# Performance work log

Measured on AMD Instinct MI355X. Metric: run time of the kernel, lower is better.

Reference implementation:

```python
import jax, jax.numpy as jnp
import numpy as np

D_MODEL = 256
D_INNER = 512
D_STATE = 16
DT_RANK = 16
D_CONV = 4
N_LAYERS = 2
EPS = 1e-5
SEQ_LEN = 16384
IN_DIM = 32
OUT_DIM = 1


def _layernorm(x, g, b):
    m = jnp.mean(x, axis=-1, keepdims=True)
    v = jnp.mean((x - m) ** 2, axis=-1, keepdims=True)
    return (x - m) * jax.lax.rsqrt(v + EPS) * g + b


def _rmsnorm(x, w):
    return x * jax.lax.rsqrt(jnp.mean(x * x, axis=-1, keepdims=True) + EPS) * w


def _selective_scan(x, delta, A, B, C, D):
    # x, delta: (B,L,ED); A: (ED,N); B,C: (B,L,N); D: (ED,)
    dA = jnp.exp(delta[..., None] * A)                    # (B,L,ED,N)
    dBx = (delta * x)[..., None] * B[:, :, None, :]       # (B,L,ED,N)

    def comb(l, r):
        al, bl = l
        ar, br = r
        return (al * ar, bl * ar + br)

    _, hs = jax.lax.associative_scan(comb, (dA, dBx), axis=1)  # (B,L,ED,N)
    y = jnp.einsum('blen,bln->ble', hs, C) + x * D
    return y


def _mamba_block(u, rms_w, inW, convW, convB, xpW, dtW, dtB, A_log, Dp, outW):
    h = _rmsnorm(u, rms_w)
    xz = h @ inW                                   # (B,L,2*ED)
    xin, z = jnp.split(xz, 2, axis=-1)
    # depthwise causal conv1d over time
    xc = jax.lax.conv_general_dilated(
        jnp.transpose(xin, (0, 2, 1)), convW,
        window_strides=(1,), padding=[(D_CONV - 1, 0)],
        feature_group_count=D_INNER,
        dimension_numbers=('NCH', 'OIH', 'NCH')) + convB[None, :, None]
    xs = jax.nn.silu(jnp.transpose(xc, (0, 2, 1)))  # (B,L,ED)
    dbc = xs @ xpW                                  # (B,L,dt_rank+2N)
    delta = jax.nn.softplus(dbc[..., :DT_RANK] @ dtW + dtB)
    Bm = dbc[..., DT_RANK:DT_RANK + D_STATE]
    Cm = dbc[..., DT_RANK + D_STATE:]
    y = _selective_scan(xs, delta, -jnp.exp(A_log), Bm, Cm, Dp)
    out = (y * jax.nn.silu(z)) @ outW
    return u + out  # residual


def _forward(x, W_in, b_in, ln1_g, ln1_b,
             rms_w, inW, convW, convB, xpW, dtW, dtB, A_log, Dp, outW,
             ln2_g, ln2_b, W1, b1, ln3_g, ln3_b, W2, b2):
    # input_proj (dropout = identity in eval)
    h = jax.nn.gelu(_layernorm(x[0] @ W_in + b_in, ln1_g, ln1_b))
    h = h[None]  # (1,L,D)
    for i in range(N_LAYERS):
        h = _mamba_block(h, rms_w[i], inW[i], convW[i], convB[i], xpW[i],
                         dtW[i], dtB[i], A_log[i], Dp[i], outW[i])
    # output_proj
    h = _layernorm(h, ln2_g, ln2_b)
    h = jax.nn.gelu(h @ W1 + b1)
    h = _layernorm(h, ln3_g, ln3_b)
    h = jnp.tanh(h @ W2 + b2)
    return h.reshape(-1)


def setup_inputs() -> dict:
    key = jax.random.key(0)
    ks = jax.random.split(key, 16)
    s = 0.02
    A = jnp.tile(jnp.arange(1, D_STATE + 1, dtype=jnp.float32)[None, :], (D_INNER, 1))
    return {
        'x': jax.random.normal(ks[0], (1, SEQ_LEN, IN_DIM), jnp.float32),
        'W_in': s * jax.random.normal(ks[1], (IN_DIM, D_MODEL), jnp.float32),
        'b_in': jnp.zeros((D_MODEL,), jnp.float32),
        'ln1_g': jnp.ones((D_MODEL,), jnp.float32),
        'ln1_b': jnp.zeros((D_MODEL,), jnp.float32),
        'rms_w': jnp.ones((N_LAYERS, D_MODEL), jnp.float32),
        'inW': s * jax.random.normal(ks[2], (N_LAYERS, D_MODEL, 2 * D_INNER), jnp.float32),
        'convW': s * jax.random.normal(ks[3], (N_LAYERS, D_INNER, 1, D_CONV), jnp.float32),
        'convB': jnp.zeros((N_LAYERS, D_INNER), jnp.float32),
        'xpW': s * jax.random.normal(ks[4], (N_LAYERS, D_INNER, DT_RANK + 2 * D_STATE), jnp.float32),
        'dtW': s * jax.random.normal(ks[5], (N_LAYERS, DT_RANK, D_INNER), jnp.float32),
        'dtB': 0.1 * jax.random.normal(ks[6], (N_LAYERS, D_INNER), jnp.float32),
        'A_log': jnp.tile(jnp.log(A)[None], (N_LAYERS, 1, 1)),
        'Dp': jnp.ones((N_LAYERS, D_INNER), jnp.float32),
        'outW': s * jax.random.normal(ks[7], (N_LAYERS, D_INNER, D_MODEL), jnp.float32),
        'ln2_g': jnp.ones((D_MODEL,), jnp.float32),
        'ln2_b': jnp.zeros((D_MODEL,), jnp.float32),
        'W1': s * jax.random.normal(ks[8], (D_MODEL, D_MODEL // 2), jnp.float32),
        'b1': jnp.zeros((D_MODEL // 2,), jnp.float32),
        'ln3_g': jnp.ones((D_MODEL // 2,), jnp.float32),
        'ln3_b': jnp.zeros((D_MODEL // 2,), jnp.float32),
        'W2': s * jax.random.normal(ks[9], (D_MODEL // 2, OUT_DIM), jnp.float32),
        'b2': jnp.zeros((OUT_DIM,), jnp.float32),
    }


def reference(x, W_in, b_in, ln1_g, ln1_b, rms_w, inW, convW, convB, xpW,
              dtW, dtB, A_log, Dp, outW, ln2_g, ln2_b, W1, b1, ln3_g, ln3_b,
              W2, b2):
    return _forward(x, W_in, b_in, ln1_g, ln1_b, rms_w, inW, convW, convB,
                    xpW, dtW, dtB, A_log, Dp, outW, ln2_g, ln2_b, W1, b1,
                    ln3_g, ln3_b, W2, b2)
```

## Files before the change

kernel.cpp:

```cpp
#include <hip/hip_runtime.h>
#include <hip/hip_bf16.h>
#include <math.h>

#define L_SEQ 16384
#define DM 256
#define DI 512
#define DS 16
#define NCH 512
#define CHL 32
#define CLB 16

typedef __attribute__((ext_vector_type(8))) short short8v;
typedef __attribute__((ext_vector_type(4))) float f32x4;

__device__ __forceinline__ float tanh_fast(float x){
  float xc = fminf(x, 15.f);
  float t = __expf(2.f*xc);
  return (t-1.f)/(t+1.f);
}
__device__ __forceinline__ float gelu_f(float x){
  float x3 = x*x*x;
  return 0.5f*x*(1.0f + tanh_fast(0.7978845608028654f*(x + 0.044715f*x3)));
}
__device__ __forceinline__ float silu_f(float x){
  return x / (1.0f + __expf(-x));
}
__device__ __forceinline__ float softplus_f(float x){
  return fmaxf(x,0.0f) + __logf(1.0f + __expf(-fabsf(x)));
}
__device__ __forceinline__ float bf2f(unsigned short u){
  return __uint_as_float(((unsigned int)u)<<16);
}
__device__ __forceinline__ void gload16(const void* g, void* l){
  __builtin_amdgcn_global_load_lds((const __attribute__((address_space(1))) void*)g,
                                   (__attribute__((address_space(3))) void*)l, 16, 0, 0);
}

__device__ __forceinline__ void powers16(float r, float* dA){
  float r2 = r*r;
  float r4 = r2*r2;
  float r8 = r4*r4;
  dA[0]=r;        dA[1]=r2;       dA[2]=r2*r;     dA[3]=r4;
  dA[4]=r4*r;     dA[5]=r4*r2;    dA[6]=r4*dA[2]; dA[7]=r8;
  dA[8]=r8*r;     dA[9]=r8*r2;    dA[10]=r8*dA[2];dA[11]=r8*r4;
  dA[12]=r8*dA[4];dA[13]=r8*dA[5];dA[14]=r8*dA[6];dA[15]=r8*r8;
}

__global__ void k_cvtw(const float* __restrict__ inW, const float* __restrict__ outW,
                       const float* __restrict__ W1, __hip_bfloat16* __restrict__ inWt,
                       __hip_bfloat16* __restrict__ outWt, __hip_bfloat16* __restrict__ W1t){
  int idx = blockIdx.x*256 + threadIdx.x;
  if(idx < 524288){
    int layer = idx >> 18;
    int r = idx & 262143;
    int n = r >> 8, k = r & 255;
    inWt[idx] = __float2bfloat16(inW[layer*262144 + k*1024 + n]);
  } else if(idx < 786432){
    int j = idx - 524288;
    int layer = j >> 17;
    int r = j & 131071;
    int n = r >> 9, k = r & 511;
    outWt[j] = __float2bfloat16(outW[layer*131072 + k*256 + n]);
  } else if(idx < 819200){
    int j = idx - 786432;
    int n = j >> 8, k = j & 255;
    W1t[j] = __float2bfloat16(W1[k*128 + n]);
  }
}

__global__ void k_wd(const float* __restrict__ xpW, const float* __restrict__ dtW,
                     __hip_bfloat16* __restrict__ Wd_t, __hip_bfloat16* __restrict__ Wbc_t){
  int idx = blockIdx.x*256 + threadIdx.x;
  if(idx < 524288){
    int layer = idx >> 18;
    int r = idx & 262143;
    int n = r >> 9, k = r & 511;
    const float* xp = xpW + layer*512*48;
    const float* dt = dtW + layer*16*512;
    float s = 0.f;
#pragma unroll
    for(int j=0;j<16;j++) s = fmaf(xp[k*48+j], dt[j*512+n], s);
    Wd_t[idx] = __float2bfloat16(s);
  } else if(idx < 655360){
    int j2 = idx - 524288;
    int layer = j2 >> 16;
    int r = j2 & 65535;
    int n = r >> 9, k = r & 511;
    float v = (n < 32) ? xpW[layer*512*48 + k*48 + 16 + n] : 0.f;
    Wbc_t[j2] = __float2bfloat16(v);
  }
}

__global__ __launch_bounds__(256) void k_input(const float* __restrict__ x,
                        const float* __restrict__ Win, const float* __restrict__ bin,
                        const float* __restrict__ g, const float* __restrict__ b,
                        __hip_bfloat16* __restrict__ u){
  int wv = threadIdx.x>>6, lane = threadIdx.x&63;
  int r = blockIdx.x*4 + wv;
  int c0 = lane*4;
  float acc[4];
  { float4 bv = *(const float4*)&bin[c0];
    acc[0]=bv.x; acc[1]=bv.y; acc[2]=bv.z; acc[3]=bv.w; }
#pragma unroll
  for(int k=0;k<32;k++){
    float xk = x[r*32+k];
    float4 wv4 = *(const float4*)&Win[k*DM+c0];
    acc[0]=fmaf(xk,wv4.x,acc[0]); acc[1]=fmaf(xk,wv4.y,acc[1]);
    acc[2]=fmaf(xk,wv4.z,acc[2]); acc[3]=fmaf(xk,wv4.w,acc[3]);
  }
  float s = (acc[0]+acc[1])+(acc[2]+acc[3]);
  float sq = acc[0]*acc[0]+acc[1]*acc[1]+acc[2]*acc[2]+acc[3]*acc[3];
#pragma unroll
  for(int o=32;o;o>>=1){ s += __shfl_xor(s,o); sq += __shfl_xor(sq,o); }
  float mean = s*(1.0f/DM);
  float var = sq*(1.0f/DM) - mean*mean;
  float rs = rsqrtf(var+1e-5f);
  float4 gv = *(const float4*)&g[c0];
  float4 bv = *(const float4*)&b[c0];
  __hip_bfloat16 ob[4] = {
    __float2bfloat16(gelu_f((acc[0]-mean)*rs*gv.x+bv.x)),
    __float2bfloat16(gelu_f((acc[1]-mean)*rs*gv.y+bv.y)),
    __float2bfloat16(gelu_f((acc[2]-mean)*rs*gv.z+bv.z)),
    __float2bfloat16(gelu_f((acc[3]-mean)*rs*gv.w+bv.w))};
  *(uint2*)&u[r*DM+c0] = *(uint2*)ob;
}

__global__ __launch_bounds__(256) void k_rms(const __hip_bfloat16* __restrict__ u,
                      const float* __restrict__ w, __hip_bfloat16* __restrict__ o){
  int wv = threadIdx.x>>6, lane = threadIdx.x&63;
  int r = blockIdx.x*4 + wv;
  int c0 = lane*4;
  ushort4 uv = *(const ushort4*)&u[r*DM+c0];
  float v0=bf2f(uv.x), v1=bf2f(uv.y), v2=bf2f(uv.z), v3=bf2f(uv.w);
  float sq = v0*v0+v1*v1+v2*v2+v3*v3;
#pragma unroll
  for(int s=32;s;s>>=1) sq += __shfl_xor(sq,s);
  float rs = rsqrtf(sq*(1.0f/DM)+1e-5f);
  float4 wv4 = *(const float4*)&w[c0];
  __hip_bfloat16 ob[4] = {
    __float2bfloat16(v0*rs*wv4.x), __float2bfloat16(v1*rs*wv4.y),
    __float2bfloat16(v2*rs*wv4.z), __float2bfloat16(v3*rs*wv4.w)};
  *(uint2*)&o[r*DM+c0] = *(uint2*)ob;
}

__global__ __launch_bounds__(256) void k_ln(const __hip_bfloat16* __restrict__ u,
                     const float* __restrict__ g, const float* __restrict__ b,
                     __hip_bfloat16* __restrict__ o){
  int wv = threadIdx.x>>6, lane = threadIdx.x&63;
  int r = blockIdx.x*4 + wv;
  int c0 = lane*4;
  ushort4 uv = *(const ushort4*)&u[r*DM+c0];
  float v[4] = {bf2f(uv.x), bf2f(uv.y), bf2f(uv.z), bf2f(uv.w)};
  float s = (v[0]+v[1])+(v[2]+v[3]);
  float sq = v[0]*v[0]+v[1]*v[1]+v[2]*v[2]+v[3]*v[3];
#pragma unroll
  for(int o2=32;o2;o2>>=1){ s += __shfl_xor(s,o2); sq += __shfl_xor(sq,o2); }
  float mean = s*(1.0f/DM);
  float var = sq*(1.0f/DM) - mean*mean;
  float rs = rsqrtf(var+1e-5f);
  float4 gv = *(const float4*)&g[c0];
  float4 bv = *(const float4*)&b[c0];
  __hip_bfloat16 ob[4] = {
    __float2bfloat16((v[0]-mean)*rs*gv.x+bv.x),
    __float2bfloat16((v[1]-mean)*rs*gv.y+bv.y),
    __float2bfloat16((v[2]-mean)*rs*gv.z+bv.z),
    __float2bfloat16((v[3]-mean)*rs*gv.w+bv.w)};
  *(uint2*)&o[r*DM+c0] = *(uint2*)ob;
}

template<int EPI, typename OT>
__global__ __launch_bounds__(512) void k_mgemm(const __hip_bfloat16* __restrict__ A,
    const __hip_bfloat16* __restrict__ Wt, const float* __restrict__ bias,
    const OT* __restrict__ R, OT* __restrict__ C, int M, int K, int ldc, int Nout){
  __shared__ char lds[69632];
  short* As = (short*)lds;
  short* Bs = (short*)(lds + 32768);
  float* Ob = (float*)lds;
  int t = threadIdx.x, lane = t&63, wave = t>>6;
  int gx = gridDim.x;
  int f = blockIdx.y*gx + blockIdx.x;
  int s = f >> 3;
  int sy = s/gx;
  int yb = (f&7)*(gridDim.y>>3) + sy;
  int xb = s - sy*gx;
  int m0 = yb*128, n0 = xb*128;
  int wm = (wave>>1)*32, wn = (wave&1)*64;
  f32x4 acc[2][4] = {};
  int nk = K >> 7;
  for(int ki=0; ki<nk; ki++){
    int kt = ki<<7;
    __syncthreads();
#pragma unroll
    for(int c=0;c<4;c++){
      int off = c*8192 + t*16;
      int row = off>>8;
      int sl  = ((off>>4)&15) ^ (row&15);
      gload16(&A [(m0+row)*K + kt + sl*8], (char*)As + off);
      gload16(&Wt[(n0+row)*K + kt + sl*8], (char*)Bs + off);
    }
    asm volatile("s_waitcnt vmcnt(0)" ::: "memory");
    __syncthreads();
#pragma unroll
    for(int ks=0; ks<4; ks++){
      short8v a[2], b[4];
      int k8 = ks*4 + (lane>>4);
#pragma unroll
      for(int i=0;i<2;i++){
        int lr = wm + i*16 + (lane&15);
        a[i] = *(const short8v*)&As[lr*128 + (k8 ^ (lr&15))*8];
      }
#pragma unroll
      for(int j=0;j<4;j++){
        int lr = wn + j*16 + (lane&15);
        b[j] = *(const short8v*)&Bs[lr*128 + (k8 ^ (lr&15))*8];
      }
#pragma unroll
      for(int i=0;i<2;i++)
#pragma unroll
        for(int j=0;j<4;j++)
          acc[i][j] = __builtin_amdgcn_mfma_f32_16x16x32_bf16(a[i], b[j], acc[i][j], 0,0,0);
    }
  }
  __syncthreads();
#pragma unroll
  for(int i=0;i<2;i++){
    int r0 = wm + i*16 + (lane>>4)*4;
#pragma unroll
    for(int j=0;j<4;j++){
      int cl = wn + j*16 + (lane&15);
#pragma unroll
      for(int r=0;r<4;r++) Ob[(r0+r)*132 + cl] = acc[i][j][r];
    }
  }
  __syncthreads();
#pragma unroll
  for(int v=0; v<8; v++){
    int fidx = (t*8+v)*4;
    int row = fidx>>7, col = fidx&127;
    if(col < Nout){
      float4 o = *(const float4*)&Ob[row*132 + col];
      int grow = m0 + row, gcol = n0 + col;
      if(EPI==1){
        if constexpr(sizeof(OT)==2){
          ushort4 rv = *(const ushort4*)&R[grow*ldc+gcol];
          o.x+=bf2f(rv.x); o.y+=bf2f(rv.y); o.z+=bf2f(rv.z); o.w+=bf2f(rv.w);
        } else {
          float4 rv = *(const float4*)&R[grow*ldc+gcol];
          o.x+=rv.x; o.y+=rv.y; o.z+=rv.z; o.w+=rv.w;
        }
      }
      if(EPI==2){
        float4 bv = *(const float4*)&bias[gcol];
        o.x=gelu_f(o.x+bv.x); o.y=gelu_f(o.y+bv.y);
        o.z=gelu_f(o.z+bv.z); o.w=gelu_f(o.w+bv.w);
      }
      if(EPI==3){
        float4 bv = *(const float4*)&bias[gcol];
        o.x=softplus_f(o.x+bv.x); o.y=softplus_f(o.y+bv.y);
        o.z=softplus_f(o.z+bv.z); o.w=softplus_f(o.w+bv.w);
      }
      if constexpr(sizeof(OT)==2){
        __hip_bfloat16 ob[4] = {__float2bfloat16(o.x),__float2bfloat16(o.y),
                                __float2bfloat16(o.z),__float2bfloat16(o.w)};
        *(uint2*)&C[grow*ldc+gcol] = *(uint2*)ob;
      } else {
        *(float4*)&C[grow*ldc+gcol] = o;
      }
    }
  }
}

__global__ __launch_bounds__(256) void k_conv(const __hip_bfloat16* __restrict__ xz,
                       const float* __restrict__ cw, const float* __restrict__ cb,
                       __hip_bfloat16* __restrict__ xs_bf){
  int idx = blockIdx.x*256 + threadIdx.x;
  int cg = idx & 127, lb = idx >> 7;
  int c4 = cg*4;
  int l0 = lb*CLB;
  float w[4][4], bias[4];
#pragma unroll
  for(int j=0;j<4;j++){
    float4 wv = *(const float4*)&cw[(c4+j)*4];
    w[j][0]=wv.x; w[j][1]=wv.y; w[j][2]=wv.z; w[j][3]=wv.w;
  }
  { float4 bv = *(const float4*)&cb[c4];
    bias[0]=bv.x; bias[1]=bv.y; bias[2]=bv.z; bias[3]=bv.w; }
  float xm0[4], xm1[4], xm2[4];
#pragma unroll
  for(int j=0;j<4;j++){ xm0[j]=0.f; xm1[j]=0.f; xm2[j]=0.f; }
  if(l0 >= 3){
    ushort4 r0 = *(const ushort4*)&xz[(l0-3)*1024 + c4];
    ushort4 r1 = *(const ushort4*)&xz[(l0-2)*1024 + c4];
    ushort4 r2 = *(const ushort4*)&xz[(l0-1)*1024 + c4];
    xm0[0]=bf2f(r0.x); xm0[1]=bf2f(r0.y); xm0[2]=bf2f(r0.z); xm0[3]=bf2f(r0.w);
    xm1[0]=bf2f(r1.x); xm1[1]=bf2f(r1.y); xm1[2]=bf2f(r1.z); xm1[3]=bf2f(r1.w);
    xm2[0]=bf2f(r2.x); xm2[1]=bf2f(r2.y); xm2[2]=bf2f(r2.z); xm2[3]=bf2f(r2.w);
  }
#pragma unroll 4
  for(int l=l0; l<l0+CLB; l++){
    ushort4 rc = *(const ushort4*)&xz[l*1024 + c4];
    float xc[4] = {bf2f(rc.x), bf2f(rc.y), bf2f(rc.z), bf2f(rc.w)};
    __hip_bfloat16 ob[4];
#pragma unroll
    for(int j=0;j<4;j++){
      float acc = bias[j];
      acc = fmaf(xm0[j], w[j][0], acc);
      acc = fmaf(xm1[j], w[j][1], acc);
      acc = fmaf(xm2[j], w[j][2], acc);
      acc = fmaf(xc[j],  w[j][3], acc);
      ob[j] = __float2bfloat16(silu_f(acc));
    }
    *(uint2*)&xs_bf[l*DI + c4] = *(uint2*)ob;
#pragma unroll
    for(int j=0;j<4;j++){ xm0[j]=xm1[j]; xm1[j]=xm2[j]; xm2[j]=xc[j]; }
  }
}

__global__ __launch_bounds__(256) void k_scan1(const __hip_bfloat16* __restrict__ delta,
                        const __hip_bfloat16* __restrict__ xs,
                        const float* __restrict__ dbc32, const float* __restrict__ A_log,
                        float* __restrict__ Atot, float* __restrict__ Btot){
  __shared__ float bcs[CHL*32];
  int t = threadIdx.x;
  int chunk = blockIdx.x >> 1;
  int e = ((blockIdx.x & 1) << 8) + t;
  int l0 = chunk*CHL;
  ((float4*)bcs)[t] = ((const float4*)&dbc32[l0*32])[t];
  float A[16];
  {
    const float4* al = (const float4*)&A_log[e*DS];
#pragma unroll
    for(int q=0;q<4;q++){
      float4 a = al[q];
      A[q*4+0] = -__expf(a.x); A[q*4+1] = -__expf(a.y);
      A[q*4+2] = -__expf(a.z); A[q*4+3] = -__expf(a.w);
    }
  }
  bool pf = true;
#pragma unroll
  for(int n=1;n<16;n++) pf = pf && (fabsf(A[n] - (n+1)*A[0]) <= 1e-4f*fabsf(A[n]));
  float carry[16], aprod[16];
#pragma unroll
  for(int n=0;n<16;n++){ carry[n]=0.f; aprod[n]=1.f; }
  __syncthreads();
  if(pf){
    float A0 = A[0];
#pragma unroll 2
    for(int li=0; li<CHL; li++){
      int l = l0 + li;
      float d  = bf2f(*(const unsigned short*)&delta[l*DI+e]);
      float xv = bf2f(*(const unsigned short*)&xs[l*DI+e]);
      float dxv = d*xv;
      const float4* bp = (const float4*)&bcs[li*32];
      float4 b0=bp[0], b1=bp[1], b2=bp[2], b3=bp[3];
      float B[16] = {b0.x,b0.y,b0.z,b0.w, b1.x,b1.y,b1.z,b1.w,
                     b2.x,b2.y,b2.z,b2.w, b3.x,b3.y,b3.z,b3.w};
      float r = __expf(d*A0);
      float dA[16]; powers16(r, dA);
#pragma unroll
      for(int n=0;n<16;n++){
        carry[n] = fmaf(carry[n], dA[n], dxv*B[n]);
        aprod[n] *= dA[n];
      }
    }
  } else {
#pragma unroll 2
    for(int li=0; li<CHL; li++){
      int l = l0 + li;
      float d  = bf2f(*(const unsigned short*)&delta[l*DI+e]);
      float xv = bf2f(*(const unsigned short*)&xs[l*DI+e]);
      float dxv = d*xv;
      const float4* bp = (const float4*)&bcs[li*32];
      float4 b0=bp[0], b1=bp[1], b2=bp[2], b3=bp[3];
      float B[16] = {b0.x,b0.y,b0.z,b0.w, b1.x,b1.y,b1.z,b1.w,
                     b2.x,b2.y,b2.z,b2.w, b3.x,b3.y,b3.z,b3.w};
#pragma unroll
      for(int n=0;n<16;n++){
        float dA = __expf(d*A[n]);
        carry[n] = fmaf(carry[n], dA, dxv*B[n]);
        aprod[n] *= dA;
      }
    }
  }
  float4* ap = (float4*)&Atot[chunk*8192 + e*DS];
  float4* bp = (float4*)&Btot[chunk*8192 + e*DS];
#pragma unroll
  for(int q=0;q<4;q++){
    ap[q] = make_float4(aprod[q*4],aprod[q*4+1],aprod[q*4+2],aprod[q*4+3]);
    bp[q] = make_float4(carry[q*4],carry[q*4+1],carry[q*4+2],carry[q*4+3]);
  }
}

__global__ void k_scan2(const float* __restrict__ Atot, const float* __restrict__ Btot,
                        float* __restrict__ h0){
  int tg = blockIdx.x*256 + threadIdx.x;
  float carry = 0.f;
  for(int c=0;c<NCH;c++){
    float a = Atot[c*8192+tg];
    float b = Btot[c*8192+tg];
    h0[c*8192+tg] = carry;
    carry = fmaf(carry, a, b);
  }
}

__global__ __launch_bounds__(256) void k_scan3(const __hip_bfloat16* __restrict__ delta,
                        const __hip_bfloat16* __restrict__ xs,
                        const float* __restrict__ dbc32, const float* __restrict__ A_log,
                        const float* __restrict__ Dp, const float* __restrict__ h0,
                        const __hip_bfloat16* __restrict__ xz, __hip_bfloat16* __restrict__ y){
  __shared__ float bcs[CHL*32];
  int t = threadIdx.x;
  int chunk = blockIdx.x >> 1;
  int e = ((blockIdx.x & 1) << 8) + t;
  int l0 = chunk*CHL;
  ((float4*)bcs)[t] = ((const float4*)&dbc32[l0*32])[t];
  float A[16];
  {
    const float4* al = (const float4*)&A_log[e*DS];
#pragma unroll
    for(int q=0;q<4;q++){
      float4 a = al[q];
      A[q*4+0] = -__expf(a.x); A[q*4+1] = -__expf(a.y);
      A[q*4+2] = -__expf(a.z); A[q*4+3] = -__expf(a.w);
    }
  }
  bool pf = true;
#pragma unroll
  for(int n=1;n<16;n++) pf = pf && (fabsf(A[n] - (n+1)*A[0]) <= 1e-4f*fabsf(A[n]));
  float carry[16];
  {
    const float4* hp = (const float4*)&h0[chunk*8192 + e*DS];
#pragma unroll
    for(int q=0;q<4;q++){
      float4 h = hp[q];
      carry[q*4+0]=h.x; carry[q*4+1]=h.y; carry[q*4+2]=h.z; carry[q*4+3]=h.w;
    }
  }
  float Dv = Dp[e];
  __syncthreads();
  if(pf){
    float A0 = A[0];
#pragma unroll 2
    for(int li=0; li<CHL; li++){
      int l = l0 + li;
      float d  = bf2f(*(const unsigned short*)&delta[l*DI+e]);
      float xv = bf2f(*(const unsigned short*)&xs[l*DI+e]);
      float dxv = d*xv;
      const float4* bp = (const float4*)&bcs[li*32];
      float4 b0=bp[0], b1=bp[1], b2=bp[2], b3=bp[3];
      float4 c0=bp[4], c1=bp[5], c2=bp[6], c3=bp[7];
      float B[16] = {b0.x,b0.y,b0.z,b0.w, b1.x,b1.y,b1.z,b1.w,
                     b2.x,b2.y,b2.z,b2.w, b3.x,b3.y,b3.z,b3.w};
      float Cv[16] = {c0.x,c0.y,c0.z,c0.w, c1.x,c1.y,c1.z,c1.w,
                      c2.x,c2.y,c2.z,c2.w, c3.x,c3.y,c3.z,c3.w};
      float r = __expf(d*A0);
      float dA[16]; powers16(r, dA);
      float p[4] = {0.f,0.f,0.f,0.f};
#pragma unroll
      for(int n=0;n<16;n++){
        carry[n] = fmaf(carry[n], dA[n], dxv*B[n]);
        p[n&3] = fmaf(carry[n], Cv[n], p[n&3]);
      }
      float ps = (p[0]+p[1]) + (p[2]+p[3]);
      float z = bf2f(*(const unsigned short*)&xz[l*1024 + 512 + e]);
      y[l*DI+e] = __float2bfloat16(fmaf(xv, Dv, ps) * silu_f(z));
    }
  } else {
#pragma unroll 2
    for(int li=0; li<CHL; li++){
      int l = l0 + li;
      float d  = bf2f(*(const unsigned short*)&delta[l*DI+e]);
      float xv = bf2f(*(const unsigned short*)&xs[l*DI+e]);
      float dxv = d*xv;
      const float4* bp = (const float4*)&bcs[li*32];
      float4 b0=bp[0], b1=bp[1], b2=bp[2], b3=bp[3];
      float4 c0=bp[4], c1=bp[5], c2=bp[6], c3=bp[7];
      float B[16] = {b0.x,b0.y,b0.z,b0.w, b1.x,b1.y,b1.z,b1.w,
                     b2.x,b2.y,b2.z,b2.w, b3.x,b3.y,b3.z,b3.w};
      float Cv[16] = {c0.x,c0.y,c0.z,c0.w, c1.x,c1.y,c1.z,c1.w,
                      c2.x,c2.y,c2.z,c2.w, c3.x,c3.y,c3.z,c3.w};
      float p[4] = {0.f,0.f,0.f,0.f};
#pragma unroll
      for(int n=0;n<16;n++){
        float dA = __expf(d*A[n]);
        carry[n] = fmaf(carry[n], dA, dxv*B[n]);
        p[n&3] = fmaf(carry[n], Cv[n], p[n&3]);
      }
      float ps = (p[0]+p[1]) + (p[2]+p[3]);
      float z = bf2f(*(const unsigned short*)&xz[l*1024 + 512 + e]);
      y[l*DI+e] = __float2bfloat16(fmaf(xv, Dv, ps) * silu_f(z));
    }
  }
}

__global__ void k_final(const float* __restrict__ h2, const float* __restrict__ g,
                        const float* __restrict__ b, const float* __restrict__ W2,
                        const float* __restrict__ b2, float* __restrict__ out){
  int lane = threadIdx.x&63;
  int wv = threadIdx.x>>6;
  int r = blockIdx.x*4 + wv;
  float v0 = h2[r*128+lane], v1 = h2[r*128+64+lane];
  float s = v0+v1, sq = v0*v0+v1*v1;
#pragma unroll
  for(int o=32;o;o>>=1){ s += __shfl_xor(s,o); sq += __shfl_xor(sq,o); }
  float mean = s*(1.0f/128), var = sq*(1.0f/128) - mean*mean;
  float rs = rsqrtf(var+1e-5f);
  float n0 = (v0-mean)*rs*g[lane]+b[lane];
  float n1 = (v1-mean)*rs*g[lane+64]+b[lane+64];
  float d = n0*W2[lane] + n1*W2[lane+64];
#pragma unroll
  for(int o=32;o;o>>=1) d += __shfl_xor(d,o);
  if(lane==0) out[r] = tanhf(d + b2[0]);
}

extern "C" void kernel_launch(void* const* d_in, const int* in_sizes, int n_in,
                              void* d_out, int out_size, void* d_ws, size_t ws_size,
                              hipStream_t stream){
  const float* x    = (const float*)d_in[0];
  const float* Win  = (const float*)d_in[1];
  const float* bin  = (const float*)d_in[2];
  const float* ln1g = (const float*)d_in[3];
  const float* ln1b = (const float*)d_in[4];
  const float* rmsw = (const float*)d_in[5];
  const float* inW  = (const float*)d_in[6];
  const float* convW= (const float*)d_in[7];
  const float* convB= (const float*)d_in[8];
  const float* xpW  = (const float*)d_in[9];
  const float* dtW  = (const float*)d_in[10];
  const float* dtB  = (const float*)d_in[11];
  const float* A_log= (const float*)d_in[12];
  const float* Dp   = (const float*)d_in[13];
  const float* outW = (const float*)d_in[14];
  const float* ln2g = (const float*)d_in[15];
  const float* ln2b = (const float*)d_in[16];
  const float* W1   = (const float*)d_in[17];
  const float* b1   = (const float*)d_in[18];
  const float* ln3g = (const float*)d_in[19];
  const float* ln3b = (const float*)d_in[20];
  const float* W2   = (const float*)d_in[21];
  const float* b2   = (const float*)d_in[22];
  float* out = (float*)d_out;
  float* ws = (float*)d_ws;
  __hip_bfloat16* u_bf = (__hip_bfloat16*)ws;
  __hip_bfloat16* hn_bf = (__hip_bfloat16*)(ws + 4194304);
  __hip_bfloat16* xz_bf = (__hip_bfloat16*)(ws + 8388608);
  float* dbc32 = ws + 16777216;
  __hip_bfloat16* delta_bf = (__hip_bfloat16*)(ws + 17301504);
  __hip_bfloat16* y_bf  = (__hip_bfloat16*)(ws + 25690112);
  __hip_bfloat16* xs_bf = (__hip_bfloat16*)(ws + 29884416);
  float* Atot  = ws + 34078720;
  float* Btot  = ws + 38273024;
  float* h0    = Btot;
  float* h2    = ws;
  __hip_bfloat16* inWt   = (__hip_bfloat16*)(ws + 42467328);
  __hip_bfloat16* outWt  = (__hip_bfloat16*)(ws + 42729472);
  __hip_bfloat16* W1t    = (__hip_bfloat16*)(ws + 42860544);
  __hip_bfloat16* Wd_t   = (__hip_bfloat16*)(ws + 42876928);
  __hip_bfloat16* Wbc_t  = (__hip_bfloat16*)(ws + 43139072);

  k_cvtw<<<3200,256,0,stream>>>(inW, outW, W1, inWt, outWt, W1t);
  k_wd<<<2560,256,0,stream>>>(xpW, dtW, Wd_t, Wbc_t);
  k_input<<<L_SEQ/4,256,0,stream>>>(x,Win,bin,ln1g,ln1b,u_bf);
  for(int i=0;i<2;i++){
    k_rms<<<L_SEQ/4,256,0,stream>>>(u_bf, rmsw+i*DM, hn_bf);
    k_mgemm<0,__hip_bfloat16><<<dim3(8, L_SEQ/128),512,0,stream>>>(hn_bf, inWt+i*262144, nullptr, nullptr, xz_bf, L_SEQ, DM, 1024, 1024);
    k_conv<<<(L_SEQ/CLB)*128/256,256,0,stream>>>(xz_bf, convW+i*DI*4, convB+i*DI, xs_bf);
    k_mgemm<3,__hip_bfloat16><<<dim3(4, L_SEQ/128),512,0,stream>>>(xs_bf, Wd_t+i*262144, dtB+i*DI, nullptr, delta_bf, L_SEQ, DI, 512, 512);
    k_mgemm<0,float><<<dim3(1, L_SEQ/128),512,0,stream>>>(xs_bf, Wbc_t+i*65536, nullptr, nullptr, dbc32, L_SEQ, DI, 32, 32);
    k_scan1<<<NCH*2,256,0,stream>>>(delta_bf, xs_bf, dbc32, A_log+i*DI*DS, Atot, Btot);
    k_scan2<<<32,256,0,stream>>>(Atot, Btot, h0);
    k_scan3<<<NCH*2,256,0,stream>>>(delta_bf, xs_bf, dbc32, A_log+i*DI*DS, Dp+i*DI, h0, xz_bf, y_bf);
    k_mgemm<1,__hip_bfloat16><<<dim3(2, L_SEQ/128),512,0,stream>>>(y_bf, outWt+i*131072, nullptr, u_bf, u_bf, L_SEQ, DI, 256, 256);
  }
  k_ln<<<L_SEQ/4,256,0,stream>>>(u_bf, ln2g, ln2b, hn_bf);
  k_mgemm<2,float><<<dim3(1, L_SEQ/128),512,0,stream>>>(hn_bf, W1t, b1, nullptr, h2, L_SEQ, DM, 128, 128);
  k_final<<<L_SEQ/4,256,0,stream>>>(h2, ln3g, ln3b, W2, b2, out);
}
```

Before: 445.2 us.

## Fuse RMSNorm into in-proj GEMM via row sum-of-squares and merge delta/BC GEMMs

Removes the standalone RMSNorm kernel. The norm weight is folded into the in-projection weights, and per-row sums of squares are produced by the input kernel and by the first out-projection epilogue using atomics. The in-proj GEMM then scales each row by rsqrt. The delta and B/C projections are merged into one GEMM with a split epilogue, the two weight-prep kernels are combined, and the scan2 carry loop batches its loads in groups of eight. This trades an extra atomic pass and zero-fill against fewer kernel launches and less activation traffic.

New measurement: 413.0 us. -7.2%, faster.

```diff
diff --git a/kernel.cpp b/kernel.cpp
--- a/kernel.cpp
+++ b/kernel.cpp
@@ -46,15 +46,17 @@
   dA[12]=r8*dA[4];dA[13]=r8*dA[5];dA[14]=r8*dA[6];dA[15]=r8*r8;
 }
 
-__global__ void k_cvtw(const float* __restrict__ inW, const float* __restrict__ outW,
-                       const float* __restrict__ W1, __hip_bfloat16* __restrict__ inWt,
-                       __hip_bfloat16* __restrict__ outWt, __hip_bfloat16* __restrict__ W1t){
+__global__ void k_prep(const float* __restrict__ inW, const float* __restrict__ rmsw,
+                       const float* __restrict__ outW, const float* __restrict__ W1,
+                       const float* __restrict__ xpW, const float* __restrict__ dtW,
+                       __hip_bfloat16* __restrict__ inWt, __hip_bfloat16* __restrict__ outWt,
+                       __hip_bfloat16* __restrict__ W1t, __hip_bfloat16* __restrict__ Wdbc_t){
   int idx = blockIdx.x*256 + threadIdx.x;
   if(idx < 524288){
     int layer = idx >> 18;
     int r = idx & 262143;
     int n = r >> 8, k = r & 255;
-    inWt[idx] = __float2bfloat16(inW[layer*262144 + k*1024 + n]);
+    inWt[idx] = __float2bfloat16(inW[layer*262144 + k*1024 + n] * rmsw[layer*256+k]);
   } else if(idx < 786432){
     int j = idx - 524288;
     int layer = j >> 17;
@@ -65,36 +67,34 @@
     int j = idx - 786432;
     int n = j >> 8, k = j & 255;
     W1t[j] = __float2bfloat16(W1[k*128 + n]);
-  }
-}
-
-__global__ void k_wd(const float* __restrict__ xpW, const float* __restrict__ dtW,
-                     __hip_bfloat16* __restrict__ Wd_t, __hip_bfloat16* __restrict__ Wbc_t){
-  int idx = blockIdx.x*256 + threadIdx.x;
-  if(idx < 524288){
-    int layer = idx >> 18;
-    int r = idx & 262143;
+  } else if(idx < 1474560){
+    int j = idx - 819200;
+    int layer = j / 327680;
+    int r = j % 327680;
     int n = r >> 9, k = r & 511;
     const float* xp = xpW + layer*512*48;
-    const float* dt = dtW + layer*16*512;
-    float s = 0.f;
-#pragma unroll
-    for(int j=0;j<16;j++) s = fmaf(xp[k*48+j], dt[j*512+n], s);
-    Wd_t[idx] = __float2bfloat16(s);
-  } else if(idx < 655360){
-    int j2 = idx - 524288;
-    int layer = j2 >> 16;
-    int r = j2 & 65535;
-    int n = r >> 9, k = r & 511;
-    float v = (n < 32) ? xpW[layer*512*48 + k*48 + 16 + n] : 0.f;
-    Wbc_t[j2] = __float2bfloat16(v);
-  }
+    float v;
+    if(n < 512){
+      const float* dt = dtW + layer*16*512;
+      float s = 0.f;
+#pragma unroll
+      for(int q=0;q<16;q++) s = fmaf(xp[k*48+q], dt[q*512+n], s);
+      v = s;
+    } else if(n < 544){
+      v = xp[k*48 + 16 + (n-512)];
+    } else v = 0.f;
+    Wdbc_t[j] = __float2bfloat16(v);
+  }
+}
+
+__global__ void k_zero(float* __restrict__ p){
+  ((float4*)p)[blockIdx.x*256 + threadIdx.x] = make_float4(0.f,0.f,0.f,0.f);
 }
 
 __global__ __launch_bounds__(256) void k_input(const float* __restrict__ x,
                         const float* __restrict__ Win, const float* __restrict__ bin,
                         const float* __restrict__ g, const float* __restrict__ b,
-                        __hip_bfloat16* __restrict__ u){
+                        __hip_bfloat16* __restrict__ u, float* __restrict__ rowsq){
   int wv = threadIdx.x>>6, lane = threadIdx.x&63;
   int r = blockIdx.x*4 + wv;
   int c0 = lane*4;
@@ -117,30 +117,18 @@
   float rs = rsqrtf(var+1e-5f);
   float4 gv = *(const float4*)&g[c0];
   float4 bv = *(const float4*)&b[c0];
-  __hip_bfloat16 ob[4] = {
-    __float2bfloat16(gelu_f((acc[0]-mean)*rs*gv.x+bv.x)),
-    __float2bfloat16(gelu_f((acc[1]-mean)*rs*gv.y+bv.y)),
-    __float2bfloat16(gelu_f((acc[2]-mean)*rs*gv.z+bv.z)),
-    __float2bfloat16(gelu_f((acc[3]-mean)*rs*gv.w+bv.w))};
+  float go[4];
+  go[0] = gelu_f((acc[0]-mean)*rs*gv.x+bv.x);
+  go[1] = gelu_f((acc[1]-mean)*rs*gv.y+bv.y);
+  go[2] = gelu_f((acc[2]-mean)*rs*gv.z+bv.z);
+  go[3] = gelu_f((acc[3]-mean)*rs*gv.w+bv.w);
+  float ssq = go[0]*go[0]+go[1]*go[1]+go[2]*go[2]+go[3]*go[3];
+#pragma unroll
+  for(int o=32;o;o>>=1) ssq += __shfl_xor(ssq,o);
+  if(lane==0) rowsq[r] = ssq;
+  __hip_bfloat16 ob[4] = {__float2bfloat16(go[0]),__float2bfloat16(go[1]),
+                          __float2bfloat16(go[2]),__float2bfloat16(go[3])};
   *(uint2*)&u[r*DM+c0] = *(uint2*)ob;
-}
-
-__global__ __launch_bounds__(256) void k_rms(const __hip_bfloat16* __restrict__ u,
-                      const float* __restrict__ w, __hip_bfloat16* __restrict__ o){
-  int wv = threadIdx.x>>6, lane = threadIdx.x&63;
-  int r = blockIdx.x*4 + wv;
-  int c0 = lane*4;
-  ushort4 uv = *(const ushort4*)&u[r*DM+c0];
-  float v0=bf2f(uv.x), v1=bf2f(uv.y), v2=bf2f(uv.z), v3=bf2f(uv.w);
-  float sq = v0*v0+v1*v1+v2*v2+v3*v3;
-#pragma unroll
-  for(int s=32;s;s>>=1) sq += __shfl_xor(sq,s);
-  float rs = rsqrtf(sq*(1.0f/DM)+1e-5f);
-  float4 wv4 = *(const float4*)&w[c0];
-  __hip_bfloat16 ob[4] = {
-    __float2bfloat16(v0*rs*wv4.x), __float2bfloat16(v1*rs*wv4.y),
-    __float2bfloat16(v2*rs*wv4.z), __float2bfloat16(v3*rs*wv4.w)};
-  *(uint2*)&o[r*DM+c0] = *(uint2*)ob;
 }
 
 __global__ __launch_bounds__(256) void k_ln(const __hip_bfloat16* __restrict__ u,
@@ -171,7 +159,8 @@
 template<int EPI, typename OT>
 __global__ __launch_bounds__(512) void k_mgemm(const __hip_bfloat16* __restrict__ A,
     const __hip_bfloat16* __restrict__ Wt, const float* __restrict__ bias,
-    const OT* __restrict__ R, OT* __restrict__ C, int M, int K, int ldc, int Nout){
+    const OT* __restrict__ R, OT* __restrict__ C, float* __restrict__ C2,
+    float* __restrict__ rowsq, int M, int K, int ldc, int Nout){
   __shared__ char lds[69632];
   short* As = (short*)lds;
   short* Bs = (short*)(lds + 32768);
@@ -233,6 +222,9 @@
     }
   }
   __syncthreads();
+  float ssq_acc = 0.f;
+  int rowq = t>>2;
+  int growq = m0 + rowq;
 #pragma unroll
   for(int v=0; v<8; v++){
     int fidx = (t*8+v)*4;
@@ -240,7 +232,7 @@
     if(col < Nout){
       float4 o = *(const float4*)&Ob[row*132 + col];
       int grow = m0 + row, gcol = n0 + col;
-      if(EPI==1){
+      if(EPI==1 || EPI==5){
         if constexpr(sizeof(OT)==2){
           ushort4 rv = *(const ushort4*)&R[grow*ldc+gcol];
           o.x+=bf2f(rv.x); o.y+=bf2f(rv.y); o.z+=bf2f(rv.z); o.w+=bf2f(rv.w);
@@ -248,25 +240,43 @@
           float4 rv = *(const float4*)&R[grow*ldc+gcol];
           o.x+=rv.x; o.y+=rv.y; o.z+=rv.z; o.w+=rv.w;
         }
+        if(EPI==5) ssq_acc += o.x*o.x + o.y*o.y + o.z*o.z + o.w*o.w;
       }
       if(EPI==2){
         float4 bv = *(const float4*)&bias[gcol];
         o.x=gelu_f(o.x+bv.x); o.y=gelu_f(o.y+bv.y);
         o.z=gelu_f(o.z+bv.z); o.w=gelu_f(o.w+bv.w);
       }
-      if(EPI==3){
-        float4 bv = *(const float4*)&bias[gcol];
-        o.x=softplus_f(o.x+bv.x); o.y=softplus_f(o.y+bv.y);
-        o.z=softplus_f(o.z+bv.z); o.w=softplus_f(o.w+bv.w);
-      }
-      if constexpr(sizeof(OT)==2){
-        __hip_bfloat16 ob[4] = {__float2bfloat16(o.x),__float2bfloat16(o.y),
-                                __float2bfloat16(o.z),__float2bfloat16(o.w)};
-        *(uint2*)&C[grow*ldc+gcol] = *(uint2*)ob;
+      if(EPI==6){
+        float rs = rsqrtf(rowsq[grow]*(1.0f/DM) + 1e-5f);
+        o.x*=rs; o.y*=rs; o.z*=rs; o.w*=rs;
+      }
+      if(EPI==4){
+        if(gcol < 512){
+          float4 bv = *(const float4*)&bias[gcol];
+          float4 so = {softplus_f(o.x+bv.x), softplus_f(o.y+bv.y),
+                       softplus_f(o.z+bv.z), softplus_f(o.w+bv.w)};
+          __hip_bfloat16 ob[4] = {__float2bfloat16(so.x),__float2bfloat16(so.y),
+                                  __float2bfloat16(so.z),__float2bfloat16(so.w)};
+          *(uint2*)&C[grow*ldc+gcol] = *(uint2*)ob;
+        } else {
+          *(float4*)&C2[grow*32 + (gcol-512)] = o;
+        }
       } else {
-        *(float4*)&C[grow*ldc+gcol] = o;
-      }
-    }
+        if constexpr(sizeof(OT)==2){
+          __hip_bfloat16 ob[4] = {__float2bfloat16(o.x),__float2bfloat16(o.y),
+                                  __float2bfloat16(o.z),__float2bfloat16(o.w)};
+          *(uint2*)&C[grow*ldc+gcol] = *(uint2*)ob;
+        } else {
+          *(float4*)&C[grow*ldc+gcol] = o;
+        }
+      }
+    }
+  }
+  if(EPI==5){
+    ssq_acc += __shfl_xor(ssq_acc,1);
+    ssq_acc += __shfl_xor(ssq_acc,2);
+    if((lane&3)==0) atomicAdd(&rowsq[growq], ssq_acc);
   }
 }
 
@@ -395,11 +405,18 @@
                         float* __restrict__ h0){
   int tg = blockIdx.x*256 + threadIdx.x;
   float carry = 0.f;
-  for(int c=0;c<NCH;c++){
-    float a = Atot[c*8192+tg];
-    float b = Btot[c*8192+tg];
-    h0[c*8192+tg] = carry;
-    carry = fmaf(carry, a, b);
+  for(int c0=0;c0<NCH;c0+=8){
+    float a[8], b[8];
+#pragma unroll
+    for(int j=0;j<8;j++){
+      a[j] = Atot[(c0+j)*8192+tg];
+      b[j] = Btot[(c0+j)*8192+tg];
+    }
+#pragma unroll
+    for(int j=0;j<8;j++){
+      h0[(c0+j)*8192+tg] = carry;
+      carry = fmaf(carry, a[j], b[j]);
+    }
   }
 }
 
@@ -542,7 +559,9 @@
   float* out = (float*)d_out;
   float* ws = (float*)d_ws;
   __hip_bfloat16* u_bf = (__hip_bfloat16*)ws;
-  __hip_bfloat16* hn_bf = (__hip_bfloat16*)(ws + 4194304);
+  float* rowsq0 = ws + 4194304;
+  float* rowsq1 = ws + 4194304 + 16384;
+  __hip_bfloat16* hn_bf = (__hip_bfloat16*)(ws + 4259840);
   __hip_bfloat16* xz_bf = (__hip_bfloat16*)(ws + 8388608);
   float* dbc32 = ws + 16777216;
   __hip_bfloat16* delta_bf = (__hip_bfloat16*)(ws + 17301504);
@@ -555,24 +574,31 @@
   __hip_bfloat16* inWt   = (__hip_bfloat16*)(ws + 42467328);
   __hip_bfloat16* outWt  = (__hip_bfloat16*)(ws + 42729472);
   __hip_bfloat16* W1t    = (__hip_bfloat16*)(ws + 42860544);
-  __hip_bfloat16* Wd_t   = (__hip_bfloat16*)(ws + 42876928);
-  __hip_bfloat16* Wbc_t  = (__hip_bfloat16*)(ws + 43139072);
-
-  k_cvtw<<<3200,256,0,stream>>>(inW, outW, W1, inWt, outWt, W1t);
-  k_wd<<<2560,256,0,stream>>>(xpW, dtW, Wd_t, Wbc_t);
-  k_input<<<L_SEQ/4,256,0,stream>>>(x,Win,bin,ln1g,ln1b,u_bf);
+  __hip_bfloat16* Wdbc_t = (__hip_bfloat16*)(ws + 42876928);
+
+  k_prep<<<5760,256,0,stream>>>(inW, rmsw, outW, W1, xpW, dtW, inWt, outWt, W1t, Wdbc_t);
+  k_zero<<<16,256,0,stream>>>(rowsq1);
+  k_input<<<L_SEQ/4,256,0,stream>>>(x,Win,bin,ln1g,ln1b,u_bf,rowsq0);
   for(int i=0;i<2;i++){
-    k_rms<<<L_SEQ/4,256,0,stream>>>(u_bf, rmsw+i*DM, hn_bf);
-    k_mgemm<0,__hip_bfloat16><<<dim3(8, L_SEQ/128),512,0,stream>>>(hn_bf, inWt+i*262144, nullptr, nullptr, xz_bf, L_SEQ, DM, 1024, 1024);
+    float* rsq_in = (i==0) ? rowsq0 : rowsq1;
+    k_mgemm<6,__hip_bfloat16><<<dim3(8, L_SEQ/128),512,0,stream>>>(
+        u_bf, inWt+i*262144, nullptr, nullptr, xz_bf, nullptr, rsq_in, L_SEQ, DM, 1024, 1024);
     k_conv<<<(L_SEQ/CLB)*128/256,256,0,stream>>>(xz_bf, convW+i*DI*4, convB+i*DI, xs_bf);
-    k_mgemm<3,__hip_bfloat16><<<dim3(4, L_SEQ/128),512,0,stream>>>(xs_bf, Wd_t+i*262144, dtB+i*DI, nullptr, delta_bf, L_SEQ, DI, 512, 512);
-    k_mgemm<0,float><<<dim3(1, L_SEQ/128),512,0,stream>>>(xs_bf, Wbc_t+i*65536, nullptr, nullptr, dbc32, L_SEQ, DI, 32, 32);
+    k_mgemm<4,__hip_bfloat16><<<dim3(5, L_SEQ/128),512,0,stream>>>(
+        xs_bf, Wdbc_t+i*327680, dtB+i*DI, nullptr, delta_bf, dbc32, nullptr, L_SEQ, DI, 512, 544);
     k_scan1<<<NCH*2,256,0,stream>>>(delta_bf, xs_bf, dbc32, A_log+i*DI*DS, Atot, Btot);
     k_scan2<<<32,256,0,stream>>>(Atot, Btot, h0);
     k_scan3<<<NCH*2,256,0,stream>>>(delta_bf, xs_bf, dbc32, A_log+i*DI*DS, Dp+i*DI, h0, xz_bf, y_bf);
-    k_mgemm<1,__hip_bfloat16><<<dim3(2, L_SEQ/128),512,0,stream>>>(y_bf, outWt+i*131072, nullptr, u_bf, u_bf, L_SEQ, DI, 256, 256);
+    if(i==0){
+      k_mgemm<5,__hip_bfloat16><<<dim3(2, L_SEQ/128),512,0,stream>>>(
+          y_bf, outWt, nullptr, u_bf, u_bf, nullptr, rowsq1, L_SEQ, DI, 256, 256);
+    } else {
+      k_mgemm<1,__hip_bfloat16><<<dim3(2, L_SEQ/128),512,0,stream>>>(
+          y_bf, outWt+131072, nullptr, u_bf, u_bf, nullptr, nullptr, L_SEQ, DI, 256, 256);
+    }
   }
   k_ln<<<L_SEQ/4,256,0,stream>>>(u_bf, ln2g, ln2b, hn_bf);
-  k_mgemm<2,float><<<dim3(1, L_SEQ/128),512,0,stream>>>(hn_bf, W1t, b1, nullptr, h2, L_SEQ, DM, 128, 128);
+  k_mgemm<2,float><<<dim3(1, L_SEQ/128),512,0,stream>>>(
+      hn_bf, W1t, b1, nullptr, h2, nullptr, nullptr, L_SEQ, DM, 128, 128);
   k_final<<<L_SEQ/4,256,0,stream>>>(h2, ln3g, ln3b, W2, b2, out);
 }
```
